# Kernel optimization log

Measured on AMD Instinct MI355X. Metric: run time of the kernel, lower is better.

## Reference

```python
import jax, jax.numpy as jnp
import numpy as np

D_MODEL = 1024
D_STATE = 16
D_CONV = 4
EXPAND = 2
D_INNER = EXPAND * D_MODEL          # 2048
DT_RANK = D_MODEL // 16             # 64
BATCH, SEQ = 4, 2048


def setup_inputs() -> dict:
    key = jax.random.key(0)
    ks = jax.random.split(key, 8)
    s = lambda k, shape, sc=0.02: jax.random.normal(k, shape, jnp.float32) * sc
    x = jax.random.normal(ks[0], (BATCH, SEQ, D_MODEL), jnp.float32)
    tau = jax.random.uniform(ks[1], (BATCH, SEQ), jnp.float32) * 7200.0  # seconds
    # S4D-real init for A
    A_log = jnp.log(jnp.broadcast_to(jnp.arange(1, D_STATE + 1, dtype=jnp.float32), (D_INNER, D_STATE)))
    return dict(
        x=x, tau=tau,
        ln_g=jnp.ones((D_MODEL,), jnp.float32),
        ln_b=jnp.zeros((D_MODEL,), jnp.float32),
        in_proj_w=s(ks[2], (2 * D_INNER, D_MODEL)),
        conv_w=s(ks[3], (D_INNER, 1, D_CONV), 0.1),   # depthwise [O, I/g=1, K]
        conv_b=jnp.zeros((D_INNER,), jnp.float32),
        x_proj_w=s(ks[4], (DT_RANK + 2 * D_STATE, D_INNER)),
        dt_proj_w=s(ks[5], (D_INNER, DT_RANK), 0.1),
        dt_proj_b=jnp.full((D_INNER,), -4.6, jnp.float32),  # softplus ~ 0.01
        A_log=A_log,
        D=jnp.ones((D_INNER,), jnp.float32),
        out_proj_w=s(ks[6], (D_MODEL, D_INNER)),
        log_decay=jnp.full((D_MODEL,), -3.0, jnp.float32),
    )


def _mamba_block(x, tau, ln_g, ln_b, in_proj_w, conv_w, conv_b, x_proj_w,
                 dt_proj_w, dt_proj_b, A_log, D, out_proj_w, log_decay):
    # LayerNorm(d_model)
    mu = jnp.mean(x, axis=-1, keepdims=True)
    var = jnp.var(x, axis=-1, keepdims=True)
    xn = (x - mu) * jax.lax.rsqrt(var + 1e-5) * ln_g + ln_b

    # in_proj -> split into conv branch and gate branch, each [B, L, d_inner]
    xz = jnp.einsum('bld,ed->ble', xn, in_proj_w)
    x_in, z = jnp.split(xz, 2, axis=-1)

    # causal depthwise conv1d over time
    xc = jax.lax.conv_general_dilated(
        x_in.transpose(0, 2, 1), conv_w, (1,), [(D_CONV - 1, 0)],
        dimension_numbers=('NCH', 'OIH', 'NCH'), feature_group_count=D_INNER)
    u = jax.nn.silu(xc.transpose(0, 2, 1) + conv_b)          # [B, L, d_inner]

    # input-dependent SSM params
    x_dbl = jnp.einsum('ble,fe->blf', u, x_proj_w)
    dt, Bm, Cm = jnp.split(x_dbl, [DT_RANK, DT_RANK + D_STATE], axis=-1)
    delta = jax.nn.softplus(jnp.einsum('blr,dr->bld', dt, dt_proj_w) + dt_proj_b)
    A = -jnp.exp(A_log)                                       # [d_inner, d_state]

    # selective scan: h_t = exp(dt*A)*h + dt*u*B_t ; y_t = <h_t, C_t>
    def step(h, inp):
        d_t, B_t, C_t, u_t = inp                              # [B,d],[B,n],[B,n],[B,d]
        h = jnp.exp(d_t[..., None] * A) * h + (d_t * u_t)[..., None] * B_t[:, None, :]
        return h, jnp.einsum('bdn,bn->bd', h, C_t)

    h0 = jnp.zeros((x.shape[0], D_INNER, D_STATE), x.dtype)
    xs = (delta.transpose(1, 0, 2), Bm.transpose(1, 0, 2),
          Cm.transpose(1, 0, 2), u.transpose(1, 0, 2))
    _, ys = jax.lax.scan(step, h0, xs)
    y = ys.transpose(1, 0, 2) + u * D
    y = y * jax.nn.silu(z)
    h_out = jnp.einsum('ble,de->bld', y, out_proj_w)          # mamba output [B,L,d_model]

    # ZOH time-decay gate + residual (dropout = identity in eval)
    tau_h = jnp.maximum(tau / 3600.0, 1e-4)[..., None]
    gate = jnp.exp(-jax.nn.softplus(log_decay) * tau_h)
    return x + h_out * gate


def reference(x, tau, ln_g, ln_b, in_proj_w, conv_w, conv_b, x_proj_w,
              dt_proj_w, dt_proj_b, A_log, D, out_proj_w, log_decay):
    return _mamba_block(x, tau, ln_g, ln_b, in_proj_w, conv_w, conv_b, x_proj_w,
                        dt_proj_w, dt_proj_b, A_log, D, out_proj_w, log_decay)
```

## Files before the change

### kernel.cpp

```cpp
#include <hip/hip_runtime.h>

typedef unsigned short u16;
typedef unsigned int u32;
typedef short s16x8 __attribute__((ext_vector_type(8)));
typedef u16 u16x8 __attribute__((ext_vector_type(8)));
typedef float f32x4 __attribute__((ext_vector_type(4)));

#define TOK 8192
#define DM 1024
#define DI 2048
#define DS 16
#define DR 64
#define NCHUNK 64
#define CH 32
#define XPN 96
#define XP_SPLIT 4
#define CONV_T 16

#define SBAR() do { asm volatile("" ::: "memory"); __builtin_amdgcn_s_barrier(); asm volatile("" ::: "memory"); } while (0)
#define WAITVM(N) do { asm volatile("s_waitcnt vmcnt(" #N ")" ::: "memory"); __builtin_amdgcn_sched_barrier(0); } while (0)
#define WAITLGKM0() do { asm volatile("s_waitcnt lgkmcnt(0)" ::: "memory"); __builtin_amdgcn_sched_barrier(0); } while (0)

__device__ __forceinline__ u16 f2bf(float f) {
    u32 u = __float_as_uint(f);
    u32 r = (u + 0x7fffu + ((u >> 16) & 1u)) >> 16;
    return (u16)r;
}
__device__ __forceinline__ float bf2f(u16 h) {
    return __uint_as_float(((u32)h) << 16);
}
__device__ __forceinline__ float softplus_f(float x) {
    return (x > 15.f) ? x : __logf(1.f + __expf(x));
}
__device__ __forceinline__ void unpack8(const uint4 v, float* o) {
    o[0] = __uint_as_float(v.x << 16); o[1] = __uint_as_float(v.x & 0xffff0000u);
    o[2] = __uint_as_float(v.y << 16); o[3] = __uint_as_float(v.y & 0xffff0000u);
    o[4] = __uint_as_float(v.z << 16); o[5] = __uint_as_float(v.z & 0xffff0000u);
    o[6] = __uint_as_float(v.w << 16); o[7] = __uint_as_float(v.w & 0xffff0000u);
}
__device__ __forceinline__ void async16(u16* lds, const u16* g) {
    __builtin_amdgcn_global_load_lds(
        (const __attribute__((address_space(1))) void*)g,
        (__attribute__((address_space(3))) void*)lds, 16, 0, 0);
}

__global__ __launch_bounds__(256) void cvt_all(
    const float* __restrict__ in_w, const float* __restrict__ xp_w,
    const float* __restrict__ dt_w, const float* __restrict__ out_w,
    const float* __restrict__ tau, const float* __restrict__ log_decay,
    u16* __restrict__ wi, u16* __restrict__ wxp, u16* __restrict__ wdt,
    u16* __restrict__ wout, float* __restrict__ th, float* __restrict__ sd) {
    const int b = blockIdx.x;
    const float* src; u16* dst; int i;
    if (b < 4096)      { src = in_w;  dst = wi;   i = b * 256 + threadIdx.x; }
    else if (b < 4288) { src = xp_w;  dst = wxp;  i = (b - 4096) * 256 + threadIdx.x; }
    else if (b < 4416) { src = dt_w;  dst = wdt;  i = (b - 4288) * 256 + threadIdx.x; }
    else if (b < 6464) { src = out_w; dst = wout; i = (b - 4416) * 256 + threadIdx.x; }
    else {
        int j = (b - 6464) * 256 + threadIdx.x;
        if (j < TOK) th[j] = fmaxf(tau[j] * (1.f / 3600.f), 1e-4f);
        if (j < DM)  sd[j] = softplus_f(log_decay[j]);
        return;
    }
    float4 v = ((const float4*)src)[i];
    ushort4 o;
    o.x = f2bf(v.x); o.y = f2bf(v.y); o.z = f2bf(v.z); o.w = f2bf(v.w);
    ((ushort4*)dst)[i] = o;
}

__global__ __launch_bounds__(256) void ln_kernel(const float* __restrict__ x,
                                                 const float* __restrict__ g,
                                                 const float* __restrict__ bb,
                                                 u16* __restrict__ xn) {
    const int tok = blockIdx.x;
    const float4 v = ((const float4*)(x + (size_t)tok * DM))[threadIdx.x];
    float s = v.x + v.y + v.z + v.w;
    float sq = v.x * v.x + v.y * v.y + v.z * v.z + v.w * v.w;
#pragma unroll
    for (int off = 32; off; off >>= 1) {
        s += __shfl_xor(s, off);
        sq += __shfl_xor(sq, off);
    }
    __shared__ float red[8];
    const int wv = threadIdx.x >> 6;
    if ((threadIdx.x & 63) == 0) { red[wv] = s; red[4 + wv] = sq; }
    __syncthreads();
    s = red[0] + red[1] + red[2] + red[3];
    sq = red[4] + red[5] + red[6] + red[7];
    const float mean = s * (1.f / DM);
    const float var = sq * (1.f / DM) - mean * mean;
    const float rstd = rsqrtf(var + 1e-5f);
    const float4 gv = ((const float4*)g)[threadIdx.x];
    const float4 bv = ((const float4*)bb)[threadIdx.x];
    ushort4 o;
    o.x = f2bf((v.x - mean) * rstd * gv.x + bv.x);
    o.y = f2bf((v.y - mean) * rstd * gv.y + bv.y);
    o.z = f2bf((v.z - mean) * rstd * gv.z + bv.z);
    o.w = f2bf((v.w - mean) * rstd * gv.w + bv.w);
    ((ushort4*)(xn + (size_t)tok * DM))[threadIdx.x] = o;
}

__global__ __launch_bounds__(512) void gemm256(
    const u16* __restrict__ A, int lda,
    const u16* __restrict__ W, int ldw, int K,
    u16* __restrict__ Cxi, u16* __restrict__ Cz) {
    __shared__ __align__(16) u16 lds[2 * 32768];
    const int tid = threadIdx.x;
    const int wave = tid >> 6, lane = tid & 63;
    const int wm = wave >> 2, wn = wave & 3;
    const int fl = lane & 15, fh = lane >> 4;
    const int swz = ((int)blockIdx.x & 7) * 64 + ((int)blockIdx.x >> 3);
    const int rg = swz >> 4, wi_ = swz & 15;
    const int bm = (rg >> 2) * 4 + (wi_ >> 2);
    const int bn = (rg & 3) * 4 + (wi_ & 3);
    const int NT = K >> 6;

    const int r0 = tid >> 3;
    const int cb = ((tid & 7) ^ (r0 & 7)) << 3;
    const int rA = bm * 256 + r0;
    const int rB = bn * 256 + r0 + (r0 & ~31);

    f32x4 acc[8][4];
#pragma unroll
    for (int m = 0; m < 8; m++)
#pragma unroll
        for (int n = 0; n < 4; n++) acc[m][n] = f32x4{0.f, 0.f, 0.f, 0.f};

    auto stageA = [&](int buf, int h, int k0) {
#pragma unroll
        for (int j = 0; j < 2; j++)
            async16(lds + buf * 32768 + h * 8192 + j * 4096 + tid * 8,
                    A + (size_t)(rA + j * 128 + h * 64) * lda + k0 + cb);
    };
    auto stageB = [&](int buf, int h, int k0) {
#pragma unroll
        for (int j = 0; j < 2; j++)
            async16(lds + buf * 32768 + 16384 + h * 8192 + j * 4096 + tid * 8,
                    W + (size_t)(rB + j * 128 + h * 32) * ldw + k0 + cb);
    };
    auto rdA = [&](int buf, int mf, int kk) -> s16x8 {
        int r = wm * 64 + (mf & 3) * 16 + fl;
        int slot = ((kk << 2) | fh) ^ (fl & 7);
        return *(const s16x8*)(lds + buf * 32768 + (mf >> 2) * 8192 + r * 64 + slot * 8);
    };
    auto rdB = [&](int buf, int nh, int nf, int kk) -> s16x8 {
        int r = wn * 32 + nf * 16 + fl;
        int slot = ((kk << 2) | fh) ^ (fl & 7);
        return *(const s16x8*)(lds + buf * 32768 + 16384 + nh * 8192 + r * 64 + slot * 8);
    };

    stageA(0, 0, 0); stageA(0, 1, 0); stageB(0, 0, 0); stageB(0, 1, 0);
    stageA(1, 0, 64); stageB(1, 0, 64); stageB(1, 1, 64);
    WAITVM(6);
    SBAR();

    for (int t = 0; t < NT; ++t) {
        const int cur = t & 1, nxt = cur ^ 1;
        const int k2 = (t + 2) << 6;
        s16x8 ah[4][2], bh0[2][2], bh1[2][2];
#pragma unroll
        for (int mf = 0; mf < 4; mf++) { ah[mf][0] = rdA(cur, mf, 0); ah[mf][1] = rdA(cur, mf, 1); }
#pragma unroll
        for (int nf = 0; nf < 2; nf++) { bh0[nf][0] = rdB(cur, 0, nf, 0); bh0[nf][1] = rdB(cur, 0, nf, 1); }
        if (t + 1 < NT) stageA(nxt, 1, (t + 1) << 6);
        SBAR();
        WAITLGKM0();
        __builtin_amdgcn_s_setprio(1);
#pragma unroll
        for (int kk = 0; kk < 2; kk++)
#pragma unroll
            for (int mf = 0; mf < 4; mf++)
#pragma unroll
                for (int nf = 0; nf < 2; nf++)
                    acc[mf][nf] = __builtin_amdgcn_mfma_f32_16x16x32_bf16(ah[mf][kk], bh0[nf][kk], acc[mf][nf], 0, 0, 0);
        __builtin_amdgcn_s_setprio(0);
        __builtin_amdgcn_sched_barrier(0);
        SBAR();
#pragma unroll
        for (int nf = 0; nf < 2; nf++) { bh1[nf][0] = rdB(cur, 1, nf, 0); bh1[nf][1] = rdB(cur, 1, nf, 1); }
        if (t + 2 < NT) stageA(cur, 0, k2);
        SBAR();
        WAITLGKM0();
        __builtin_amdgcn_s_setprio(1);
#pragma unroll
        for (int kk = 0; kk < 2; kk++)
#pragma unroll
            for (int mf = 0; mf < 4; mf++)
#pragma unroll
                for (int nf = 0; nf < 2; nf++)
                    acc[mf][2 + nf] = __builtin_amdgcn_mfma_f32_16x16x32_bf16(ah[mf][kk], bh1[nf][kk], acc[mf][2 + nf], 0, 0, 0);
        __builtin_amdgcn_s_setprio(0);
        __builtin_amdgcn_sched_barrier(0);
        SBAR();
#pragma unroll
        for (int mf = 0; mf < 4; mf++) { ah[mf][0] = rdA(cur, 4 + mf, 0); ah[mf][1] = rdA(cur, 4 + mf, 1); }
        if (t + 2 < NT) stageB(cur, 0, k2);
        SBAR();
        WAITLGKM0();
        __builtin_amdgcn_s_setprio(1);
#pragma unroll
        for (int kk = 0; kk < 2; kk++)
#pragma unroll
            for (int mf = 0; mf < 4; mf++)
#pragma unroll
                for (int nf = 0; nf < 2; nf++)
                    acc[4 + mf][2 + nf] = __builtin_amdgcn_mfma_f32_16x16x32_bf16(ah[mf][kk], bh1[nf][kk], acc[4 + mf][2 + nf], 0, 0, 0);
        __builtin_amdgcn_s_setprio(0);
        __builtin_amdgcn_sched_barrier(0);
        SBAR();
        if (t + 2 < NT) { stageB(cur, 1, k2); WAITVM(6); }
        else           { WAITVM(0); }
        SBAR();
        __builtin_amdgcn_s_setprio(1);
#pragma unroll
        for (int kk = 0; kk < 2; kk++)
#pragma unroll
            for (int mf = 0; mf < 4; mf++)
#pragma unroll
                for (int nf = 0; nf < 2; nf++)
                    acc[4 + mf][nf] = __builtin_amdgcn_mfma_f32_16x16x32_bf16(ah[mf][kk], bh0[nf][kk], acc[4 + mf][nf], 0, 0, 0);
        __builtin_amdgcn_s_setprio(0);
        __builtin_amdgcn_sched_barrier(0);
        SBAR();
    }

    u16* dst = (bn < 8) ? Cxi : Cz;
    const int cbase = (bn < 8) ? bn * 256 : (bn - 8) * 256;
#pragma unroll
    for (int mf = 0; mf < 8; mf++)
#pragma unroll
        for (int j = 0; j < 4; j++) {
            int row = bm * 256 + wm * 128 + mf * 16 + fh * 4 + j;
#pragma unroll
            for (int n = 0; n < 4; n++) {
                int col = cbase + wn * 64 + n * 16 + fl;
                dst[(size_t)row * DI + col] = f2bf(acc[mf][n][j]);
            }
        }
}

__global__ __launch_bounds__(512) void gemm_out(
    const u16* __restrict__ A, int lda,
    const u16* __restrict__ W, int ldw, int K,
    float* __restrict__ Cf, int ldc,
    const float* __restrict__ xres, const float* __restrict__ th,
    const float* __restrict__ sd) {
    __shared__ __align__(16) u16 lds[2 * 24576];
    const int tid = threadIdx.x;
    const int wave = tid >> 6, lane = tid & 63;
    const int wm = wave >> 2, wn = wave & 3;
    const int fl = lane & 15, fh = lane >> 4;
    const int swz = ((int)blockIdx.x & 7) * 32 + ((int)blockIdx.x >> 3);
    const int rg = swz >> 3, w8 = swz & 7;
    const int bm = (rg >> 1) * 2 + (w8 >> 2);
    const int bn = (rg & 1) * 4 + (w8 & 3);
    const int NT = K >> 6;

    const int r0 = tid >> 3;
    const int cb = ((tid & 7) ^ (r0 & 7)) << 3;
    const int rA = bm * 256 + r0;
    const int rB = bn * 128 + r0;

    f32x4 acc[8][2];
#pragma unroll
    for (int m = 0; m < 8; m++)
#pragma unroll
        for (int n = 0; n < 2; n++) acc[m][n] = f32x4{0.f, 0.f, 0.f, 0.f};

    auto stageA = [&](int buf, int h, int k0) {
#pragma unroll
        for (int j = 0; j < 2; j++)
            async16(lds + buf * 24576 + h * 8192 + j * 4096 + tid * 8,
                    A + (size_t)(rA + j * 128 + h * 64) * lda + k0 + cb);
    };
    auto stageB = [&](int buf, int k0) {
#pragma unroll
        for (int j = 0; j < 2; j++)
            async16(lds + buf * 24576 + 16384 + j * 4096 + tid * 8,
                    W + (size_t)(rB + j * 64) * ldw + k0 + cb);
    };
    auto rdA = [&](int buf, int mf, int kk) -> s16x8 {
        int r = wm * 64 + (mf & 3) * 16 + fl;
        int slot = ((kk << 2) | fh) ^ (fl & 7);
        return *(const s16x8*)(lds + buf * 24576 + (mf >> 2) * 8192 + r * 64 + slot * 8);
    };
    auto rdB = [&](int buf, int nf, int kk) -> s16x8 {
        int r = wn * 32 + nf * 16 + fl;
        int slot = ((kk << 2) | fh) ^ (fl & 7);
        return *(const s16x8*)(lds + buf * 24576 + 16384 + r * 64 + slot * 8);
    };

    stageA(0, 0, 0); stageA(0, 1, 0); stageB(0, 0);
    stageA(1, 0, 64); stageB(1, 64);
    WAITVM(4);
    SBAR();

    for (int t = 0; t < NT; ++t) {
        const int cur = t & 1, nxt = cur ^ 1;
        const int k2 = (t + 2) << 6;
        s16x8 ah[4][2], bh0[2], bh1[2];
#pragma unroll
        for (int mf = 0; mf < 4; mf++) { ah[mf][0] = rdA(cur, mf, 0); ah[mf][1] = rdA(cur, mf, 1); }
        bh0[0] = rdB(cur, 0, 0); bh0[1] = rdB(cur, 0, 1);
        if (t + 1 < NT) stageA(nxt, 1, (t + 1) << 6);
        SBAR();
        WAITLGKM0();
        __builtin_amdgcn_s_setprio(1);
#pragma unroll
        for (int kk = 0; kk < 2; kk++)
#pragma unroll
            for (int mf = 0; mf < 4; mf++)
                acc[mf][0] = __builtin_amdgcn_mfma_f32_16x16x32_bf16(ah[mf][kk], bh0[kk], acc[mf][0], 0, 0, 0);
        __builtin_amdgcn_s_setprio(0);
        __builtin_amdgcn_sched_barrier(0);
        SBAR();
        bh1[0] = rdB(cur, 1, 0); bh1[1] = rdB(cur, 1, 1);
        if (t + 2 < NT) stageA(cur, 0, k2);
        SBAR();
        WAITLGKM0();
        __builtin_amdgcn_s_setprio(1);
#pragma unroll
        for (int kk = 0; kk < 2; kk++)
#pragma unroll
            for (int mf = 0; mf < 4; mf++)
                acc[mf][1] = __builtin_amdgcn_mfma_f32_16x16x32_bf16(ah[mf][kk], bh1[kk], acc[mf][1], 0, 0, 0);
        __builtin_amdgcn_s_setprio(0);
        __builtin_amdgcn_sched_barrier(0);
        SBAR();
#pragma unroll
        for (int mf = 0; mf < 4; mf++) { ah[mf][0] = rdA(cur, 4 + mf, 0); ah[mf][1] = rdA(cur, 4 + mf, 1); }
        if (t + 2 < NT) stageB(cur, k2);
        SBAR();
        WAITLGKM0();
        __builtin_amdgcn_s_setprio(1);
#pragma unroll
        for (int kk = 0; kk < 2; kk++)
#pragma unroll
            for (int mf = 0; mf < 4; mf++)
                acc[4 + mf][1] = __builtin_amdgcn_mfma_f32_16x16x32_bf16(ah[mf][kk], bh1[kk], acc[4 + mf][1], 0, 0, 0);
        __builtin_amdgcn_s_setprio(0);
        __builtin_amdgcn_sched_barrier(0);
        SBAR();
        if (t + 2 < NT) { WAITVM(4); }
        else           { WAITVM(0); }
        SBAR();
        __builtin_amdgcn_s_setprio(1);
#pragma unroll
        for (int kk = 0; kk < 2; kk++)
#pragma unroll
            for (int mf = 0; mf < 4; mf++)
                acc[4 + mf][0] = __builtin_amdgcn_mfma_f32_16x16x32_bf16(ah[mf][kk], bh0[kk], acc[4 + mf][0], 0, 0, 0);
        __builtin_amdgcn_s_setprio(0);
        __builtin_amdgcn_sched_barrier(0);
        SBAR();
    }

#pragma unroll
    for (int mf = 0; mf < 8; mf++)
#pragma unroll
        for (int j = 0; j < 4; j++) {
            int row = bm * 256 + wm * 128 + mf * 16 + fh * 4 + j;
            float t = th[row];
#pragma unroll
            for (int n = 0; n < 2; n++) {
                int col = bn * 128 + wn * 32 + n * 16 + fl;
                size_t idx = (size_t)row * ldc + col;
                Cf[idx] = xres[idx] + acc[mf][n][j] * __expf(-sd[col] * t);
            }
        }
}

__global__ __launch_bounds__(256) void gemm_bt(
    const u16* __restrict__ A, int lda,
    const u16* __restrict__ W,
    u16* __restrict__ Cb, int ldc,
    int M, int N, int K,
    const float* __restrict__ bias) {
    __shared__ u16 As[128 * 32];
    __shared__ u16 Bs[128 * 32];
    const int tid = threadIdx.x;
    const int wave = tid >> 6, lane = tid & 63;
    const int bm = blockIdx.x, bn = blockIdx.y;
    const int srow = lane >> 2, scol = (lane & 3) * 8;
    const int wr = wave >> 1, wc = wave & 1;
    const int fl = lane & 15, fh = lane >> 4;

    f32x4 acc[4][4];
#pragma unroll
    for (int m = 0; m < 4; m++)
#pragma unroll
        for (int n = 0; n < 4; n++) acc[m][n] = f32x4{0.f, 0.f, 0.f, 0.f};

    int ra[2], rb[2];
    u16* ldsA[2]; u16* ldsB[2];
#pragma unroll
    for (int i = 0; i < 2; i++) {
        int r = (wave * 2 + i) * 16 + srow;
        ra[i] = min(bm * 128 + r, M - 1);
        rb[i] = min(bn * 128 + r, N - 1);
        ldsA[i] = As + (wave * 2 + i) * 512 + lane * 8;
        ldsB[i] = Bs + (wave * 2 + i) * 512 + lane * 8;
    }

    for (int k0 = 0; k0 < K; k0 += 32) {
        __syncthreads();
#pragma unroll
        for (int i = 0; i < 2; i++) {
            async16(ldsA[i], A + (size_t)ra[i] * lda + k0 + scol);
            async16(ldsB[i], W + (size_t)rb[i] * K + k0 + scol);
        }
        __syncthreads();
        s16x8 av[4], bv[4];
#pragma unroll
        for (int m = 0; m < 4; m++)
            av[m] = *(const s16x8*)(As + (wr * 64 + m * 16 + fl) * 32 + fh * 8);
#pragma unroll
        for (int n = 0; n < 4; n++)
            bv[n] = *(const s16x8*)(Bs + (wc * 64 + n * 16 + fl) * 32 + fh * 8);
#pragma unroll
        for (int m = 0; m < 4; m++)
#pragma unroll
            for (int n = 0; n < 4; n++)
                acc[m][n] = __builtin_amdgcn_mfma_f32_16x16x32_bf16(av[m], bv[n], acc[m][n], 0, 0, 0);
    }

#pragma unroll
    for (int m = 0; m < 4; m++) {
#pragma unroll
        for (int j = 0; j < 4; j++) {
            int row = bm * 128 + wr * 64 + m * 16 + fh * 4 + j;
            if (row >= M) continue;
#pragma unroll
            for (int n = 0; n < 4; n++) {
                int col = bn * 128 + wc * 64 + n * 16 + fl;
                if (col >= N) continue;
                Cb[(size_t)row * ldc + col] = f2bf(softplus_f(acc[m][n][j] + bias[col]));
            }
        }
    }
}

__global__ __launch_bounds__(256) void xp_gemm(const u16* __restrict__ A,
                                               const u16* __restrict__ W,
                                               float* __restrict__ part) {
    __shared__ u16 As[128 * 64];
    __shared__ u16 Bs[XPN * 64];
    const int tid = threadIdx.x;
    const int wave = tid >> 6, lane = tid & 63;
    const int bm = blockIdx.x, sp = blockIdx.y;
    const int fl = lane & 15, fh = lane >> 4;
    const int trow = tid >> 3, tcol = (tid & 7) * 8;

    f32x4 acc[2][6];
#pragma unroll
    for (int m = 0; m < 2; m++)
#pragma unroll
        for (int n = 0; n < 6; n++) acc[m][n] = f32x4{0.f, 0.f, 0.f, 0.f};

    const int kbeg = sp * (DI / XP_SPLIT);
    for (int k0 = kbeg; k0 < kbeg + DI / XP_SPLIT; k0 += 64) {
        __syncthreads();
#pragma unroll
        for (int i = 0; i < 4; i++)
            async16(As + i * 2048 + tid * 8,
                    A + (size_t)(bm * 128 + i * 32 + trow) * DI + k0 + tcol);
#pragma unroll
        for (int i = 0; i < 3; i++)
            async16(Bs + i * 2048 + tid * 8,
                    W + (size_t)(i * 32 + trow) * DI + k0 + tcol);
        __syncthreads();
#pragma unroll
        for (int kk = 0; kk < 2; kk++) {
            s16x8 av[2], bv[6];
#pragma unroll
            for (int m = 0; m < 2; m++)
                av[m] = *(const s16x8*)(As + (wave * 32 + m * 16 + fl) * 64 + kk * 32 + fh * 8);
#pragma unroll
            for (int n = 0; n < 6; n++)
                bv[n] = *(const s16x8*)(Bs + (n * 16 + fl) * 64 + kk * 32 + fh * 8);
#pragma unroll
            for (int m = 0; m < 2; m++)
#pragma unroll
                for (int n = 0; n < 6; n++)
                    acc[m][n] = __builtin_amdgcn_mfma_f32_16x16x32_bf16(av[m], bv[n], acc[m][n], 0, 0, 0);
        }
    }
    float* dst = part + (size_t)sp * TOK * XPN;
#pragma unroll
    for (int m = 0; m < 2; m++)
#pragma unroll
        for (int j = 0; j < 4; j++) {
            int row = bm * 128 + wave * 32 + m * 16 + fh * 4 + j;
#pragma unroll
            for (int n = 0; n < 6; n++) {
                int col = n * 16 + fl;
                dst[(size_t)row * XPN + col] = acc[m][n][j];
            }
        }
}

__global__ __launch_bounds__(256) void xp_reduce(const float* __restrict__ part,
                                                 u16* __restrict__ out) {
    int i = blockIdx.x * 256 + threadIdx.x;
    if (i >= TOK * XPN) return;
    float s = 0.f;
#pragma unroll
    for (int sp = 0; sp < XP_SPLIT; sp++) s += part[(size_t)sp * TOK * XPN + i];
    out[i] = f2bf(s);
}

__global__ __launch_bounds__(256) void conv_silu_kernel(const u16* __restrict__ xi,
                                                        const float* __restrict__ cw,
                                                        const float* __restrict__ cb,
                                                        u16* __restrict__ u) {
    const int b = blockIdx.y;
    const int l0 = blockIdx.x * CONV_T;
    const int d0 = threadIdx.x * 8;
    float w0[8], w1[8], w2[8], w3[8], bias[8];
#pragma unroll
    for (int e = 0; e < 8; e++) {
        float4 wv = ((const float4*)cw)[d0 + e];
        w0[e] = wv.x; w1[e] = wv.y; w2[e] = wv.z; w3[e] = wv.w;
        bias[e] = cb[d0 + e];
    }
    float win[4][8];
#pragma unroll
    for (int i = 0; i < 3; i++) {
        int l = l0 - 3 + i;
        int slot = (l0 + 1 + i) & 3;
        if (l < 0) {
#pragma unroll
            for (int e = 0; e < 8; e++) win[slot][e] = 0.f;
        } else {
            u16x8 v = *(const u16x8*)(xi + ((size_t)(b * 2048 + l)) * DI + d0);
#pragma unroll
            for (int e = 0; e < 8; e++) win[slot][e] = bf2f(v[e]);
        }
    }
#pragma unroll
    for (int t = 0; t < CONV_T; t++) {
        const int l = l0 + t;
        const size_t tok = (size_t)b * 2048 + l;
        u16x8 v = *(const u16x8*)(xi + tok * DI + d0);
        const int s3 = t & 3;
#pragma unroll
        for (int e = 0; e < 8; e++) win[s3][e] = bf2f(v[e]);
        const int s0 = (t + 1) & 3, s1 = (t + 2) & 3, s2 = (t + 3) & 3;
        u16x8 o;
#pragma unroll
        for (int e = 0; e < 8; e++) {
            float a = bias[e];
            a = fmaf(w0[e], win[s0][e], a);
            a = fmaf(w1[e], win[s1][e], a);
            a = fmaf(w2[e], win[s2][e], a);
            a = fmaf(w3[e], win[s3][e], a);
            o[e] = f2bf(a / (1.f + __expf(-a)));
        }
        *(u16x8*)(u + tok * DI + d0) = o;
    }
}

__global__ __launch_bounds__(256) void scan_passA(const u16* __restrict__ delta,
                                                  const u16* __restrict__ u,
                                                  const u16* __restrict__ xdbl,
                                                  const float* __restrict__ A_log,
                                                  float* __restrict__ qh,
                                                  float* __restrict__ Sarr) {
    const int d = blockIdx.x * 256 + threadIdx.x;
    const int b = blockIdx.y, c = blockIdx.z;
    float Av[16];
#pragma unroll
    for (int n = 0; n < 16; n++) Av[n] = -__expf(A_log[d * 16 + n]);
    bool fast = true;
#pragma unroll
    for (int n = 0; n < 16; n++) fast = fast && (fabsf(Av[n] + (float)(n + 1)) < 1e-4f * (n + 1));
    const bool allfast = __all(fast);

    float h[16];
#pragma unroll
    for (int n = 0; n < 16; n++) h[n] = 0.f;
    float S = 0.f;
    const int l0 = c * CH;
    size_t tok = (size_t)b * 2048 + l0;
    float dt = bf2f(delta[tok * DI + d]);
    float uu = bf2f(u[tok * DI + d]);
    const uint4* bp0 = (const uint4*)(xdbl + tok * 96 + 64);
    uint4 b0 = bp0[0], b1 = bp0[1];
    for (int t = 0; t < CH; ++t) {
        const int tn = (t + 1 < CH) ? t + 1 : t;
        const size_t tokn = (size_t)b * 2048 + l0 + tn;
        float dt_n = bf2f(delta[tokn * DI + d]);
        float uu_n = bf2f(u[tokn * DI + d]);
        const uint4* bpn = (const uint4*)(xdbl + tokn * 96 + 64);
        uint4 b0n = bpn[0], b1n = bpn[1];
        float du = dt * uu;
        float Bv[16];
        unpack8(b0, Bv); unpack8(b1, Bv + 8);
        float e[16];
        if (allfast) {
            float r = __expf(-dt);
            e[0] = r;
#pragma unroll
            for (int n = 1; n < 16; n++) e[n] = e[n - 1] * r;
        } else {
#pragma unroll
            for (int n = 0; n < 16; n++) e[n] = __expf(dt * Av[n]);
        }
#pragma unroll
        for (int n = 0; n < 16; n++) h[n] = fmaf(e[n], h[n], du * Bv[n]);
        S += dt;
        dt = dt_n; uu = uu_n; b0 = b0n; b1 = b1n;
    }
    const size_t base = ((size_t)(c * 4 + b) * 16) * DI + d;
#pragma unroll
    for (int n = 0; n < 16; n++) qh[base + (size_t)n * DI] = h[n];
    Sarr[(size_t)(c * 4 + b) * DI + d] = S;
}

__global__ __launch_bounds__(256) void scan_passB(float* __restrict__ qh,
                                                  const float* __restrict__ Sarr,
                                                  const float* __restrict__ A_log) {
    const int idx = blockIdx.x * 256 + threadIdx.x;
    const int d = idx & (DI - 1);
    const int n = (idx >> 11) & 15;
    const int b = idx >> 15;
    const float Avn = -__expf(A_log[d * 16 + n]);
    float h = 0.f;
    for (int c = 0; c < NCHUNK; c++) {
        const size_t base = ((size_t)(c * 4 + b) * 16 + n) * DI + d;
        const float qv = qh[base];
        const float S = Sarr[(size_t)(c * 4 + b) * DI + d];
        qh[base] = h;
        h = fmaf(__expf(Avn * S), h, qv);
    }
}

__global__ __launch_bounds__(256) void scan_passC(const u16* __restrict__ delta,
                                                  const u16* __restrict__ u,
                                                  const u16* __restrict__ xdbl,
                                                  const u16* __restrict__ z,
                                                  const float* __restrict__ A_log,
                                                  const float* __restrict__ Dvec,
                                                  const float* __restrict__ qh,
                                                  u16* __restrict__ yg) {
    const int d = blockIdx.x * 256 + threadIdx.x;
    const int b = blockIdx.y, c = blockIdx.z;
    float Av[16];
#pragma unroll
    for (int n = 0; n < 16; n++) Av[n] = -__expf(A_log[d * 16 + n]);
    bool fast = true;
#pragma unroll
    for (int n = 0; n < 16; n++) fast = fast && (fabsf(Av[n] + (float)(n + 1)) < 1e-4f * (n + 1));
    const bool allfast = __all(fast);
    const float Dd = Dvec[d];

    float h[16];
    const size_t hbase = ((size_t)(c * 4 + b) * 16) * DI + d;
#pragma unroll
    for (int n = 0; n < 16; n++) h[n] = qh[hbase + (size_t)n * DI];

    const int l0 = c * CH;
    size_t tok = (size_t)b * 2048 + l0;
    float dt = bf2f(delta[tok * DI + d]);
    float uu = bf2f(u[tok * DI + d]);
    float zz = bf2f(z[tok * DI + d]);
    const uint4* bp0 = (const uint4*)(xdbl + tok * 96 + 64);
    uint4 b0 = bp0[0], b1 = bp0[1], c0 = bp0[2], c1 = bp0[3];
    for (int t = 0; t < CH; ++t) {
        const int tn = (t + 1 < CH) ? t + 1 : t;
        const size_t tokn = (size_t)b * 2048 + l0 + tn;
        float dt_n = bf2f(delta[tokn * DI + d]);
        float uu_n = bf2f(u[tokn * DI + d]);
        float zz_n = bf2f(z[tokn * DI + d]);
        const uint4* bpn = (const uint4*)(xdbl + tokn * 96 + 64);
        uint4 b0n = bpn[0], b1n = bpn[1], c0n = bpn[2], c1n = bpn[3];

        float du = dt * uu;
        float Bv[16], Cv[16];
        unpack8(b0, Bv); unpack8(b1, Bv + 8);
        unpack8(c0, Cv); unpack8(c1, Cv + 8);
        float e[16];
        if (allfast) {
            float r = __expf(-dt);
            e[0] = r;
#pragma unroll
            for (int n = 1; n < 16; n++) e[n] = e[n - 1] * r;
        } else {
#pragma unroll
            for (int n = 0; n < 16; n++) e[n] = __expf(dt * Av[n]);
        }
        float y = 0.f;
#pragma unroll
        for (int n = 0; n < 16; n++) {
            h[n] = fmaf(e[n], h[n], du * Bv[n]);
            y = fmaf(h[n], Cv[n], y);
        }
        float sz = zz / (1.f + __expf(-zz));
        const size_t tokc = (size_t)b * 2048 + l0 + t;
        yg[tokc * DI + d] = f2bf((y + uu * Dd) * sz);

        dt = dt_n; uu = uu_n; zz = zz_n;
        b0 = b0n; b1 = b1n; c0 = c0n; c1 = c1n;
    }
}

extern "C" void kernel_launch(void* const* d_in, const int* in_sizes, int n_in,
                              void* d_out, int out_size, void* d_ws, size_t ws_size,
                              hipStream_t stream) {
    const float* x = (const float*)d_in[0];
    const float* tau = (const float*)d_in[1];
    const float* ln_g = (const float*)d_in[2];
    const float* ln_b = (const float*)d_in[3];
    const float* in_proj_w = (const float*)d_in[4];
    const float* conv_w = (const float*)d_in[5];
    const float* conv_b = (const float*)d_in[6];
    const float* x_proj_w = (const float*)d_in[7];
    const float* dt_proj_w = (const float*)d_in[8];
    const float* dt_proj_b = (const float*)d_in[9];
    const float* A_log = (const float*)d_in[10];
    const float* Dvec = (const float*)d_in[11];
    const float* out_proj_w = (const float*)d_in[12];
    const float* log_decay = (const float*)d_in[13];
    float* out = (float*)d_out;

    char* ws = (char*)d_ws;
    size_t off = 0;
    auto alloc = [&](size_t bytes) -> void* {
        void* p = ws + off;
        off += (bytes + 255) & ~(size_t)255;
        return p;
    };
    u16* xn    = (u16*)alloc((size_t)TOK * DM * 2);
    u16* w_in  = (u16*)alloc((size_t)2 * DI * DM * 2);
    u16* w_xp  = (u16*)alloc((size_t)XPN * DI * 2);
    u16* w_dt  = (u16*)alloc((size_t)DI * DR * 2);
    u16* w_out = (u16*)alloc((size_t)DM * DI * 2);
    u16* xi    = (u16*)alloc((size_t)TOK * DI * 2);
    u16* z     = (u16*)alloc((size_t)TOK * DI * 2);
    u16* u     = (u16*)alloc((size_t)TOK * DI * 2);
    u16* xdbl  = (u16*)alloc((size_t)TOK * XPN * 2);
    u16* delta = (u16*)alloc((size_t)TOK * DI * 2);
    float* qh   = (float*)alloc((size_t)NCHUNK * 4 * 16 * DI * 4);
    float* Sarr = (float*)alloc((size_t)NCHUNK * 4 * DI * 4);
    u16* yg    = (u16*)alloc((size_t)TOK * DI * 2);
    float* th = (float*)alloc((size_t)TOK * 4);
    float* sd = (float*)alloc((size_t)DM * 4);
    float* xp_part = (float*)xn;

    cvt_all<<<6496, 256, 0, stream>>>(in_proj_w, x_proj_w, dt_proj_w, out_proj_w,
                                      tau, log_decay, w_in, w_xp, w_dt, w_out, th, sd);

    ln_kernel<<<TOK, 256, 0, stream>>>(x, ln_g, ln_b, xn);

    gemm256<<<512, 512, 0, stream>>>(xn, DM, w_in, DM, DM, xi, z);
    conv_silu_kernel<<<dim3(2048 / CONV_T, 4), 256, 0, stream>>>(xi, conv_w, conv_b, u);

    xp_gemm<<<dim3(64, XP_SPLIT), 256, 0, stream>>>(u, w_xp, xp_part);
    xp_reduce<<<(TOK * XPN + 255) / 256, 256, 0, stream>>>(xp_part, xdbl);

    gemm_bt<<<dim3(64, 16), 256, 0, stream>>>(xdbl, XPN, w_dt, delta, DI,
                                              TOK, DI, DR, dt_proj_b);

    scan_passA<<<dim3(8, 4, NCHUNK), 256, 0, stream>>>(delta, u, xdbl, A_log, qh, Sarr);
    scan_passB<<<512, 256, 0, stream>>>(qh, Sarr, A_log);
    scan_passC<<<dim3(8, 4, NCHUNK), 256, 0, stream>>>(delta, u, xdbl, z, A_log, Dvec, qh, yg);

    gemm_out<<<256, 512, 0, stream>>>(yg, DI, w_out, DI, DI, out, DM, x, th, sd);
}
```

Measured before the change: 308.2 us.

## Collapse four-phase GEMM main loop into two phases with all B fragments preloaded

Both bf16 MFMA GEMM kernels (in_proj and out_proj) now load every B fragment for a k-step at once. Each iteration runs two compute phases, one per A half, instead of four quadrant phases. All next-tile global staging is issued together in the second phase, which halves the barriers and LDS-wait points per iteration. The cost is more VGPRs held live for B fragments and less interleaving of global loads with MFMA work, which could hurt latency hiding or occupancy.

```diff
diff --git a/kernel.cpp b/kernel.cpp
--- a/kernel.cpp
+++ b/kernel.cpp
@@ -157,11 +157,14 @@
     for (int t = 0; t < NT; ++t) {
         const int cur = t & 1, nxt = cur ^ 1;
         const int k2 = (t + 2) << 6;
-        s16x8 ah[4][2], bh0[2][2], bh1[2][2];
+        s16x8 ah[4][2], bh[4][2];
 #pragma unroll
         for (int mf = 0; mf < 4; mf++) { ah[mf][0] = rdA(cur, mf, 0); ah[mf][1] = rdA(cur, mf, 1); }
 #pragma unroll
-        for (int nf = 0; nf < 2; nf++) { bh0[nf][0] = rdB(cur, 0, nf, 0); bh0[nf][1] = rdB(cur, 0, nf, 1); }
+        for (int nf = 0; nf < 2; nf++) {
+            bh[nf][0] = rdB(cur, 0, nf, 0); bh[nf][1] = rdB(cur, 0, nf, 1);
+            bh[2 + nf][0] = rdB(cur, 1, nf, 0); bh[2 + nf][1] = rdB(cur, 1, nf, 1);
+        }
         if (t + 1 < NT) stageA(nxt, 1, (t + 1) << 6);
         SBAR();
         WAITLGKM0();
@@ -171,14 +174,19 @@
 #pragma unroll
             for (int mf = 0; mf < 4; mf++)
 #pragma unroll
-                for (int nf = 0; nf < 2; nf++)
-                    acc[mf][nf] = __builtin_amdgcn_mfma_f32_16x16x32_bf16(ah[mf][kk], bh0[nf][kk], acc[mf][nf], 0, 0, 0);
+                for (int nf = 0; nf < 4; nf++)
+                    acc[mf][nf] = __builtin_amdgcn_mfma_f32_16x16x32_bf16(ah[mf][kk], bh[nf][kk], acc[mf][nf], 0, 0, 0);
         __builtin_amdgcn_s_setprio(0);
         __builtin_amdgcn_sched_barrier(0);
         SBAR();
 #pragma unroll
-        for (int nf = 0; nf < 2; nf++) { bh1[nf][0] = rdB(cur, 1, nf, 0); bh1[nf][1] = rdB(cur, 1, nf, 1); }
-        if (t + 2 < NT) stageA(cur, 0, k2);
+        for (int mf = 0; mf < 4; mf++) { ah[mf][0] = rdA(cur, 4 + mf, 0); ah[mf][1] = rdA(cur, 4 + mf, 1); }
+        if (t + 2 < NT) {
+            stageA(cur, 0, k2); stageB(cur, 0, k2); stageB(cur, 1, k2);
+            WAITVM(6);
+        } else {
+            WAITVM(0);
+        }
         SBAR();
         WAITLGKM0();
         __builtin_amdgcn_s_setprio(1);
@@ -187,38 +195,8 @@
 #pragma unroll
             for (int mf = 0; mf < 4; mf++)
 #pragma unroll
-                for (int nf = 0; nf < 2; nf++)
-                    acc[mf][2 + nf] = __builtin_amdgcn_mfma_f32_16x16x32_bf16(ah[mf][kk], bh1[nf][kk], acc[mf][2 + nf], 0, 0, 0);
-        __builtin_amdgcn_s_setprio(0);
-        __builtin_amdgcn_sched_barrier(0);
-        SBAR();
-#pragma unroll
-        for (int mf = 0; mf < 4; mf++) { ah[mf][0] = rdA(cur, 4 + mf, 0); ah[mf][1] = rdA(cur, 4 + mf, 1); }
-        if (t + 2 < NT) stageB(cur, 0, k2);
-        SBAR();
-        WAITLGKM0();
-        __builtin_amdgcn_s_setprio(1);
-#pragma unroll
-        for (int kk = 0; kk < 2; kk++)
-#pragma unroll
-            for (int mf = 0; mf < 4; mf++)
-#pragma unroll
-                for (int nf = 0; nf < 2; nf++)
-                    acc[4 + mf][2 + nf] = __builtin_amdgcn_mfma_f32_16x16x32_bf16(ah[mf][kk], bh1[nf][kk], acc[4 + mf][2 + nf], 0, 0, 0);
-        __builtin_amdgcn_s_setprio(0);
-        __builtin_amdgcn_sched_barrier(0);
-        SBAR();
-        if (t + 2 < NT) { stageB(cur, 1, k2); WAITVM(6); }
-        else           { WAITVM(0); }
-        SBAR();
-        __builtin_amdgcn_s_setprio(1);
-#pragma unroll
-        for (int kk = 0; kk < 2; kk++)
-#pragma unroll
-            for (int mf = 0; mf < 4; mf++)
-#pragma unroll
-                for (int nf = 0; nf < 2; nf++)
-                    acc[4 + mf][nf] = __builtin_amdgcn_mfma_f32_16x16x32_bf16(ah[mf][kk], bh0[nf][kk], acc[4 + mf][nf], 0, 0, 0);
+                for (int nf = 0; nf < 4; nf++)
+                    acc[4 + mf][nf] = __builtin_amdgcn_mfma_f32_16x16x32_bf16(ah[mf][kk], bh[nf][kk], acc[4 + mf][nf], 0, 0, 0);
         __builtin_amdgcn_s_setprio(0);
         __builtin_amdgcn_sched_barrier(0);
         SBAR();
@@ -298,10 +276,11 @@
     for (int t = 0; t < NT; ++t) {
         const int cur = t & 1, nxt = cur ^ 1;
         const int k2 = (t + 2) << 6;
-        s16x8 ah[4][2], bh0[2], bh1[2];
+        s16x8 ah[4][2], bh[2][2];
 #pragma unroll
         for (int mf = 0; mf < 4; mf++) { ah[mf][0] = rdA(cur, mf, 0); ah[mf][1] = rdA(cur, mf, 1); }
-        bh0[0] = rdB(cur, 0, 0); bh0[1] = rdB(cur, 0, 1);
+#pragma unroll
+        for (int nf = 0; nf < 2; nf++) { bh[nf][0] = rdB(cur, nf, 0); bh[nf][1] = rdB(cur, nf, 1); }
         if (t + 1 < NT) stageA(nxt, 1, (t + 1) << 6);
         SBAR();
         WAITLGKM0();
@@ -310,12 +289,20 @@
         for (int kk = 0; kk < 2; kk++)
 #pragma unroll
             for (int mf = 0; mf < 4; mf++)
-                acc[mf][0] = __builtin_amdgcn_mfma_f32_16x16x32_bf16(ah[mf][kk], bh0[kk], acc[mf][0], 0, 0, 0);
+#pragma unroll
+                for (int nf = 0; nf < 2; nf++)
+                    acc[mf][nf] = __builtin_amdgcn_mfma_f32_16x16x32_bf16(ah[mf][kk], bh[nf][kk], acc[mf][nf], 0, 0, 0);
         __builtin_amdgcn_s_setprio(0);
         __builtin_amdgcn_sched_barrier(0);
         SBAR();
-        bh1[0] = rdB(cur, 1, 0); bh1[1] = rdB(cur, 1, 1);
-        if (t + 2 < NT) stageA(cur, 0, k2);
+#pragma unroll
+        for (int mf = 0; mf < 4; mf++) { ah[mf][0] = rdA(cur, 4 + mf, 0); ah[mf][1] = rdA(cur, 4 + mf, 1); }
+        if (t + 2 < NT) {
+            stageA(cur, 0, k2); stageB(cur, k2);
+            WAITVM(4);
+        } else {
+            WAITVM(0);
+        }
         SBAR();
         WAITLGKM0();
         __builtin_amdgcn_s_setprio(1);
@@ -323,33 +310,9 @@
         for (int kk = 0; kk < 2; kk++)
 #pragma unroll
             for (int mf = 0; mf < 4; mf++)
-                acc[mf][1] = __builtin_amdgcn_mfma_f32_16x16x32_bf16(ah[mf][kk], bh1[kk], acc[mf][1], 0, 0, 0);
-        __builtin_amdgcn_s_setprio(0);
-        __builtin_amdgcn_sched_barrier(0);
-        SBAR();
-#pragma unroll
-        for (int mf = 0; mf < 4; mf++) { ah[mf][0] = rdA(cur, 4 + mf, 0); ah[mf][1] = rdA(cur, 4 + mf, 1); }
-        if (t + 2 < NT) stageB(cur, k2);
-        SBAR();
-        WAITLGKM0();
-        __builtin_amdgcn_s_setprio(1);
-#pragma unroll
-        for (int kk = 0; kk < 2; kk++)
-#pragma unroll
-            for (int mf = 0; mf < 4; mf++)
-                acc[4 + mf][1] = __builtin_amdgcn_mfma_f32_16x16x32_bf16(ah[mf][kk], bh1[kk], acc[4 + mf][1], 0, 0, 0);
-        __builtin_amdgcn_s_setprio(0);
-        __builtin_amdgcn_sched_barrier(0);
-        SBAR();
-        if (t + 2 < NT) { WAITVM(4); }
-        else           { WAITVM(0); }
-        SBAR();
-        __builtin_amdgcn_s_setprio(1);
-#pragma unroll
-        for (int kk = 0; kk < 2; kk++)
-#pragma unroll
-            for (int mf = 0; mf < 4; mf++)
-                acc[4 + mf][0] = __builtin_amdgcn_mfma_f32_16x16x32_bf16(ah[mf][kk], bh0[kk], acc[4 + mf][0], 0, 0, 0);
+#pragma unroll
+                for (int nf = 0; nf < 2; nf++)
+                    acc[4 + mf][nf] = __builtin_amdgcn_mfma_f32_16x16x32_bf16(ah[mf][kk], bh[nf][kk], acc[4 + mf][nf], 0, 0, 0);
         __builtin_amdgcn_s_setprio(0);
         __builtin_amdgcn_sched_barrier(0);
         SBAR();
```

Measured after the change: 304.3 us. No clear change (-1.3%).
